# Performance work log

Hardware: AMD Instinct MI355X
Metric: run time of the kernel (lower is better)

The kernel has to match this reference:

```python
import jax, jax.numpy as jnp
import numpy as np

B, Q, C, H, W, E, HID_ATT, HID_MLP, NUM_CLASSES, NUM_LABELS = 8, 64, 512, 16, 16, 512, 128, 512, 14, 64


def setup_inputs() -> dict:
    key = jax.random.key(0)
    ks = jax.random.split(key, 16)
    s = 0.02
    return {
        "feature": jax.random.normal(ks[0], (B, C, H, W), jnp.float32),
        "label_ids": jax.random.randint(ks[1], (B, Q), 0, NUM_LABELS),
        "query_table": jax.random.normal(ks[2], (NUM_LABELS, E), jnp.float32) * s,
        "W_film": jax.random.normal(ks[3], (E, 2 * C), jnp.float32) * s,
        "b_film": jnp.zeros((2 * C,), jnp.float32),
        "W_att_h": jax.random.normal(ks[4], (C, HID_ATT), jnp.float32) * s,
        "b_att_h": jnp.zeros((HID_ATT,), jnp.float32),
        "W_att_f": jax.random.normal(ks[5], (HID_ATT, 1), jnp.float32) * s,
        "b_att_f": jnp.zeros((1,), jnp.float32),
        "W_mlp1": jax.random.normal(ks[6], (C, HID_MLP), jnp.float32) * s,
        "b_mlp1": jnp.zeros((HID_MLP,), jnp.float32),
        "W_mlp2": jax.random.normal(ks[7], (HID_MLP, NUM_CLASSES), jnp.float32) * s,
        "b_mlp2": jnp.zeros((NUM_CLASSES,), jnp.float32),
    }


def gelu(x):
    return jax.nn.gelu(x, approximate=False)  # torch default GELU is exact erf


def reference(feature, label_ids, query_table, W_film, b_film, W_att_h, b_att_h,
              W_att_f, b_att_f, W_mlp1, b_mlp1, W_mlp2, b_mlp2):
    # query embedding lookup: (B, Q, E)
    qe = query_table[label_ids]
    # flatten spatial: (B, HW, C)
    f = feature.reshape(feature.shape[0], feature.shape[1], -1).transpose(0, 2, 1)
    # FiLM params from queries: (B, Q, 2C) -> gamma, beta (B, Q, C)
    gb = jnp.einsum("bqe,ec->bqc", qe, W_film) + b_film
    gamma, beta = jnp.split(gb, 2, axis=-1)
    # FiLM-modulated features: (B, Q, HW, C)
    film = f[:, None, :, :] * gamma[:, :, None, :] + beta[:, :, None, :]
    # local attention MLP -> sigmoid gate (B, Q, HW, 1)
    hidden = gelu(jnp.einsum("bqnc,ch->bqnh", film, W_att_h) + b_att_h)
    attn = jax.nn.sigmoid(jnp.einsum("bqnh,ho->bqno", hidden, W_att_f) + b_att_f)
    # weighted sum pool over HW, normalized by attention mass
    pooled = (attn * film).sum(axis=2) / (attn.sum(axis=2) + 1e-8)  # (B, Q, C)
    # classification MLP
    logits = jnp.einsum("bqh,ho->bqo", gelu(jnp.einsum("bqc,ch->bqh", pooled, W_mlp1) + b_mlp1), W_mlp2) + b_mlp2
    return logits  # (B, Q, NUM_CLASSES)
```

## Files before the change

kernel.cpp:

```cpp
#include <hip/hip_runtime.h>
#include <hip/hip_bf16.h>

#define B_    8
#define Q_    64
#define C_    512
#define HW_   256
#define E_    512
#define HATT_ 128
#define HMLP_ 512
#define NCLS_ 14
#define NLAB_ 64

typedef unsigned short u16;
typedef unsigned int   u32;
typedef __attribute__((ext_vector_type(8))) short short8;
typedef __attribute__((ext_vector_type(4))) float f32x4;


__device__ __forceinline__ float gelu_fast(float x) {
    const float ax = fabsf(x);
    const float t  = __builtin_amdgcn_rcpf(1.0f + 0.3275911f * ax);
    const float p  = t * (0.254829592f +
                     t * (-0.284496736f +
                     t * (1.421413741f +
                     t * (-1.453152027f +
                     t * 1.061405429f))));
    const float e  = __expf(-x * x);
    const float er = copysignf(1.0f - p * e, x);
    return 0.5f * x * (1.0f + er);
}
__device__ __forceinline__ float sigmoid_(float x) {
    return 1.0f / (1.0f + __expf(-x));
}
__device__ __forceinline__ u16 f2bf(float x) {
    u32 u = __float_as_uint(x);
    u32 r = (u + 0x7fffu + ((u >> 16) & 1u)) >> 16;
    return (u16)r;
}
__device__ __forceinline__ float bf2f(u16 u) {
    return __uint_as_float(((u32)u) << 16);
}
__device__ __forceinline__ void gl2lds16(const void* gsrc, void* ldsdst) {
    __builtin_amdgcn_global_load_lds(
        (const __attribute__((address_space(1))) u32*)gsrc,
        (__attribute__((address_space(3))) u32*)ldsdst, 16, 0, 0);
}

__global__ __launch_bounds__(256) void prep_misc(
    const float* __restrict__ qt, const float* __restrict__ W_film,
    const float* __restrict__ feature, const float* __restrict__ W_mlp1,
    const int* __restrict__ label_ids,
    float* __restrict__ GBp, u16* __restrict__ W1bf, u16* __restrict__ fT,
    int* __restrict__ perm) {

    __shared__ __align__(16) char sm[16896];
    const int bid = blockIdx.x, t = threadIdx.x;

    if (bid < 256) {
        float* qrow = (float*)sm;
        const int l = bid >> 2, cq = bid & 3;
        if (t < 128) qrow[t] = qt[l * E_ + cq * 128 + t];
        __syncthreads();
        const float* wp = W_film + (size_t)(cq * 128) * 1024 + t * 4;
        f32x4 a = {0.f, 0.f, 0.f, 0.f};
        #pragma unroll 8
        for (int c = 0; c < 128; ++c) {
            const float4 w = *(const float4*)(wp + (size_t)c * 1024);
            const float q = qrow[c];
            a.x += q * w.x; a.y += q * w.y; a.z += q * w.z; a.w += q * w.w;
        }
        *(f32x4*)&GBp[(size_t)bid * 1024 + t * 4] = a;
    } else if (bid < 512) {
        float (*tile)[65] = (float(*)[65])sm;
        const int bb = bid - 256;
        const int b = bb >> 5, c0 = ((bb >> 2) & 7) * 64, n0 = (bb & 3) * 64;
        const float* fb = feature + (size_t)b * C_ * HW_;
        const int cl = t >> 2, nq = t & 3;
        #pragma unroll
        for (int i = 0; i < 4; ++i) {
            float4 v = *(const float4*)&fb[(c0 + cl) * HW_ + n0 + nq * 16 + i * 4];
            tile[cl][nq * 16 + i * 4 + 0] = v.x;
            tile[cl][nq * 16 + i * 4 + 1] = v.y;
            tile[cl][nq * 16 + i * 4 + 2] = v.z;
            tile[cl][nq * 16 + i * 4 + 3] = v.w;
        }
        __syncthreads();
        const int nl = t >> 2, cqq = t & 3;
        u16 pk[16];
        #pragma unroll
        for (int k = 0; k < 16; ++k) pk[k] = f2bf(tile[cqq * 16 + k][nl]);
        u16* dst = fT + (size_t)(b * HW_ + n0 + nl) * C_ + c0 + cqq * 16;
        *(uint4*)dst       = *(uint4*)pk;
        *(uint4*)(dst + 8) = *(uint4*)(pk + 8);
    } else if (bid < 576) {
        const int b2 = bid - 512;
        #pragma unroll
        for (int k = 0; k < 2; ++k) {
            const int idx = (b2 * 512 + k * 256 + t) * 8;
            float4 v0 = *(const float4*)&W_mlp1[idx];
            float4 v1 = *(const float4*)&W_mlp1[idx + 4];
            u16 pk[8] = {f2bf(v0.x), f2bf(v0.y), f2bf(v0.z), f2bf(v0.w),
                         f2bf(v1.x), f2bf(v1.y), f2bf(v1.z), f2bf(v1.w)};
            *(uint4*)&W1bf[idx] = *(uint4*)pk;
        }
    } else {
        int* cnt = (int*)sm;
        if (t < 64) cnt[t] = 0;
        __syncthreads();
        const int l0 = label_ids[t], l1 = label_ids[t + 256];
        atomicAdd(&cnt[l0], 1);
        atomicAdd(&cnt[l1], 1);
        __syncthreads();
        if (t == 0) {
            int run = 0;
            for (int i = 0; i < 64; ++i) { const int c = cnt[i]; cnt[i] = run; run += c; }
        }
        __syncthreads();
        const int p0 = atomicAdd(&cnt[l0], 1);
        perm[p0] = t | (l0 << 16);
        const int p1 = atomicAdd(&cnt[l1], 1);
        perm[p1] = (t + 256) | (l1 << 16);
    }
}

__global__ __launch_bounds__(256) void prep_wg(
    const float* __restrict__ b_film, const float* __restrict__ W_att_h,
    const float* __restrict__ GBp,
    float* __restrict__ Gl, float* __restrict__ Bl,
    u16* __restrict__ WgT, float* __restrict__ Dlp) {

    __shared__ float g_s[128], b_s[128], dred[256];
    const int bid = blockIdx.x, t = threadIdx.x;
    const int l = bid >> 2, cq = bid & 3;

    if (t < 128) {
        const int c = cq * 128 + t;
        float g = b_film[c], be = b_film[512 + c];
        #pragma unroll
        for (int j = 0; j < 4; ++j) {
            g  += GBp[(size_t)(l * 4 + j) * 1024 + c];
            be += GBp[(size_t)(l * 4 + j) * 1024 + 512 + c];
        }
        g_s[t] = g; b_s[t] = be;
        Gl[l * C_ + c] = g;
        Bl[l * C_ + c] = be;
    }
    __syncthreads();

    const int h = t & 127, ch = t >> 7;
    const int s = cq * 2 + ch;
    char* dst = (char*)WgT + (size_t)l * 131072 + s * 16384 + h * 128;
    float dl = 0.f;
    #pragma unroll
    for (int g = 0; g < 8; ++g) {
        u16 pk[8];
        #pragma unroll
        for (int j = 0; j < 8; ++j) {
            const int cl = ch * 64 + g * 8 + j;
            const float w = W_att_h[(size_t)(cq * 128 + cl) * HATT_ + h];
            pk[j] = f2bf(g_s[cl] * w);
            dl += b_s[cl] * w;
        }
        *(uint4*)(dst + ((g ^ (h & 7)) * 16)) = *(uint4*)pk;
    }
    dred[t] = dl;
    __syncthreads();
    if (t < 128)
        Dlp[(size_t)(l * 4 + cq) * 128 + t] = dred[t] + dred[128 + t];
}

__global__ __launch_bounds__(512, 4) void attn_gemm(
    const float* __restrict__ W_att_f, const float* __restrict__ b_att_f,
    const float* __restrict__ b_att_h, const float* __restrict__ Dlp,
    const int*   __restrict__ perm,    const u16* __restrict__ WgT,
    const u16*   __restrict__ fT,
    float* __restrict__ pP, float* __restrict__ pA) {

    __shared__ __align__(16) char Ash[32768];
    __shared__ __align__(16) char Bsh[16384];
    __shared__ float d_s[HATT_];
    __shared__ float wf_s[HATT_];
    __shared__ float attn_part[2][HW_];
    __shared__ float attn_s[HW_];

    const int t = threadIdx.x;
    const int srank = (blockIdx.x & 7) * 64 + (blockIdx.x >> 3);
    const int pe = perm[srank];
    const int bq = pe & 0xffff, l = pe >> 16;
    const int b = bq >> 6;

    if (t < HATT_) {
        d_s[t] = b_att_h[t]
               + Dlp[(size_t)(l * 4 + 0) * 128 + t]
               + Dlp[(size_t)(l * 4 + 1) * 128 + t]
               + Dlp[(size_t)(l * 4 + 2) * 128 + t]
               + Dlp[(size_t)(l * 4 + 3) * 128 + t];
        wf_s[t] = W_att_f[t];
    }

    const u16* fTb = fT + (size_t)b * HW_ * C_;
    const u16* Wl  = WgT + (size_t)l * 65536;

    const int an  = t >> 3;
    const int asl = (t & 7) ^ (an & 7);

    #define STAGE(s_) {                                                       \
        _Pragma("unroll")                                                     \
        for (int it = 0; it < 4; ++it)                                        \
            gl2lds16(fTb + (size_t)(it * 64 + an) * C_ + (s_) * 64 + asl * 8, \
                     Ash + (it * 512 + t) * 16);                              \
        _Pragma("unroll")                                                     \
        for (int it = 0; it < 2; ++it)                                        \
            gl2lds16(Wl + (size_t)(s_) * 8192 + (size_t)(it * 512 + t) * 8,   \
                     Bsh + (it * 512 + t) * 16);                              \
    }

    const int lane = t & 63, w = t >> 6;
    const int wm = w >> 1, wc = w & 1;
    const int lr = lane & 15, lk = lane >> 4;

    const f32x4 zero = {0.f, 0.f, 0.f, 0.f};
    f32x4 acc[4][4];
    #pragma unroll
    for (int mi = 0; mi < 4; ++mi)
        #pragma unroll
        for (int ni = 0; ni < 4; ++ni) acc[mi][ni] = zero;

    STAGE(0);
    __syncthreads();

    for (int s = 0; s < 8; ++s) {
        #pragma unroll
        for (int ks = 0; ks < 2; ++ks) {
            const int slot = ks * 4 + lk;
            short8 af[4], bf[4];
            #pragma unroll
            for (int mi = 0; mi < 4; ++mi) {
                const int nl = wm * 64 + mi * 16 + lr;
                af[mi] = *(const short8*)(Ash + nl * 128 + ((slot ^ (nl & 7)) * 16));
            }
            #pragma unroll
            for (int ni = 0; ni < 4; ++ni) {
                const int h = wc * 64 + ni * 16 + lr;
                bf[ni] = *(const short8*)(Bsh + h * 128 + ((slot ^ (h & 7)) * 16));
            }
            #pragma unroll
            for (int mi = 0; mi < 4; ++mi)
                #pragma unroll
                for (int ni = 0; ni < 4; ++ni)
                    acc[mi][ni] = __builtin_amdgcn_mfma_f32_16x16x32_bf16(
                        af[mi], bf[ni], acc[mi][ni], 0, 0, 0);
        }
        if (s < 7) {
            __syncthreads();
            STAGE(s + 1);
        }
        __syncthreads();
    }

    #pragma unroll
    for (int mi = 0; mi < 4; ++mi) {
        #pragma unroll
        for (int j = 0; j < 4; ++j) {
            float sum = 0.f;
            #pragma unroll
            for (int ni = 0; ni < 4; ++ni) {
                const int h = wc * 64 + ni * 16 + lr;
                sum += gelu_fast(acc[mi][ni][j] + d_s[h]) * wf_s[h];
            }
            sum += __shfl_xor(sum, 1);
            sum += __shfl_xor(sum, 2);
            sum += __shfl_xor(sum, 4);
            sum += __shfl_xor(sum, 8);
            if (lr == 0) attn_part[wc][wm * 64 + mi * 16 + lk * 4 + j] = sum;
        }
    }
    __syncthreads();
    if (t < HW_)
        attn_s[t] = sigmoid_(attn_part[0][t] + attn_part[1][t] + b_att_f[0]);
    __syncthreads();
    if (t < 64) {
        float a = attn_s[t] + attn_s[t + 64] + attn_s[t + 128] + attn_s[t + 192];
        #pragma unroll
        for (int m = 1; m < 64; m <<= 1) a += __shfl_xor(a, m);
        if (t == 0) pA[bq] = a;
    }

    float* pred = (float*)Ash;
    {
        const int ng = t >> 7, cb = (t & 127) * 4;
        const u16* fp = fTb + cb;
        f32x4 p = zero;
        #pragma unroll 8
        for (int n = ng * 64; n < ng * 64 + 64; ++n) {
            const uint2 v = *(const uint2*)(fp + (size_t)n * C_);
            const float a = attn_s[n];
            p.x += a * __uint_as_float(v.x << 16);
            p.y += a * __uint_as_float(v.x & 0xffff0000u);
            p.z += a * __uint_as_float(v.y << 16);
            p.w += a * __uint_as_float(v.y & 0xffff0000u);
        }
        *(f32x4*)&pred[ng * 512 + cb] = p;
    }
    __syncthreads();
    pP[(size_t)bq * C_ + t] = pred[t] + pred[512 + t] + pred[1024 + t] + pred[1536 + t];
}

__global__ __launch_bounds__(512) void mlp_head(
    const int*   __restrict__ label_ids,
    const float* __restrict__ Gl, const float* __restrict__ Bl,
    const float* __restrict__ b_mlp1, const float* __restrict__ W_mlp2,
    const float* __restrict__ b_mlp2, const float* __restrict__ pP,
    const float* __restrict__ pA,     const u16* __restrict__ W1bf,
    float* __restrict__ out) {

    __shared__ float pooled_s[2][C_];
    __shared__ float zred[2][2][HMLP_];
    __shared__ float z_s[2][HMLP_];
    __shared__ float red_s[32 * NCLS_];

    const int t = threadIdx.x;
    const int bq0 = blockIdx.x * 2;

    {
        const int bqi = t >> 8, cc = (t & 255) * 2;
        const int bq = bq0 + bqi, l = label_ids[bq];
        const float A = pA[bq];
        const float inv = 1.0f / (A + 1e-8f);
        #pragma unroll
        for (int i = 0; i < 2; ++i) {
            const int c = cc + i;
            const float p = pP[(size_t)bq * C_ + c];
            pooled_s[bqi][c] = (Gl[l * C_ + c] * p + Bl[l * C_ + c] * A) * inv;
        }
    }
    __syncthreads();

    {
        const int hp = t & 255, cg = t >> 8;
        float z00 = 0.f, z01 = 0.f, z10 = 0.f, z11 = 0.f;
        const u16* wp = W1bf + hp * 2;
        #pragma unroll 8
        for (int c = cg * 256; c < cg * 256 + 256; ++c) {
            const u32 v = *(const u32*)(wp + (size_t)c * HMLP_);
            const float w0 = __uint_as_float(v << 16);
            const float w1 = __uint_as_float(v & 0xffff0000u);
            const float pa = pooled_s[0][c], pb = pooled_s[1][c];
            z00 += pa * w0; z01 += pa * w1;
            z10 += pb * w0; z11 += pb * w1;
        }
        float2 a0 = {z00, z01}, a1 = {z10, z11};
        *(float2*)&zred[cg][0][hp * 2] = a0;
        *(float2*)&zred[cg][1][hp * 2] = a1;
    }
    __syncthreads();
    {
        const int bqi = t >> 8, h2 = (t & 255) * 2;
        #pragma unroll
        for (int i = 0; i < 2; ++i) {
            const int h = h2 + i;
            z_s[bqi][h] = gelu_fast(zred[0][bqi][h] + zred[1][bqi][h] + b_mlp1[h]);
        }
    }
    __syncthreads();

    #pragma unroll
    for (int bqi = 0; bqi < 2; ++bqi) {
        if (t < 448) {
            const int o = t % 14, seg = t / 14;
            float s = 0.f;
            #pragma unroll
            for (int k = 0; k < 16; ++k) {
                const int h = seg * 16 + k;
                s += z_s[bqi][h] * W_mlp2[h * NCLS_ + o];
            }
            red_s[seg * NCLS_ + o] = s;
        }
        __syncthreads();
        if (t < NCLS_) {
            float s = b_mlp2[t];
            #pragma unroll
            for (int seg = 0; seg < 32; ++seg) s += red_s[seg * NCLS_ + t];
            out[(bq0 + bqi) * NCLS_ + t] = s;
        }
        __syncthreads();
    }
}

extern "C" void kernel_launch(void* const* d_in, const int* in_sizes, int n_in,
                              void* d_out, int out_size, void* d_ws, size_t ws_size,
                              hipStream_t stream) {
    const float* feature   = (const float*)d_in[0];
    const int*   label_ids = (const int*)  d_in[1];
    const float* qt        = (const float*)d_in[2];
    const float* W_film    = (const float*)d_in[3];
    const float* b_film    = (const float*)d_in[4];
    const float* W_att_h   = (const float*)d_in[5];
    const float* b_att_h   = (const float*)d_in[6];
    const float* W_att_f   = (const float*)d_in[7];
    const float* b_att_f   = (const float*)d_in[8];
    const float* W_mlp1    = (const float*)d_in[9];
    const float* b_mlp1    = (const float*)d_in[10];
    const float* W_mlp2    = (const float*)d_in[11];
    const float* b_mlp2    = (const float*)d_in[12];
    float* out = (float*)d_out;

    char* wsb   = (char*)d_ws;
    float* GBp  = (float*)wsb;
    float* pP   = (float*)wsb;
    float* pA   = (float*)(wsb + 1048576);
    int*   perm = (int*)  (wsb + 1050624);
    float* Dlp  = (float*)(wsb + 1052672);
    float* Gl   = (float*)(wsb + 1183744);
    float* Bl   = (float*)(wsb + 1314816);
    u16*   W1bf = (u16*)  (wsb + 1445888);
    u16*   fTp  = (u16*)  (wsb + 1970176);
    u16*   WgT  = (u16*)  (wsb + 4067328);

    hipLaunchKernelGGL(prep_misc, dim3(577), dim3(256), 0, stream,
                       qt, W_film, feature, W_mlp1, label_ids,
                       GBp, W1bf, fTp, perm);
    hipLaunchKernelGGL(prep_wg, dim3(256), dim3(256), 0, stream,
                       b_film, W_att_h, GBp, Gl, Bl, WgT, Dlp);
    hipLaunchKernelGGL(attn_gemm, dim3(512), dim3(512), 0, stream,
                       W_att_f, b_att_f, b_att_h, Dlp, perm, WgT, fTp, pP, pA);
    hipLaunchKernelGGL(mlp_head, dim3(256), dim3(512), 0, stream,
                       label_ids, Gl, Bl, b_mlp1, W_mlp2, b_mlp2,
                       pP, pA, W1bf, out);
}
```

Before: 67.94 us.

## Double-buffer attention GEMM LDS tiles with 32-wide K stages

Splits the K dimension into 16 stages of 32 instead of 8 stages of 64 and double-buffers the A and B LDS tiles. The next stage's global-to-LDS copy is issued before the current stage's MFMAs, so loads can overlap compute and one barrier per stage is dropped. The weight pre-pack kernel is rewritten to the matching 64-byte row layout with a new XOR swizzle. This adds more barriers overall and smaller per-stage work, and the new swizzle may change LDS bank-conflict behaviour.

```diff
diff --git a/kernel.cpp b/kernel.cpp
--- a/kernel.cpp
+++ b/kernel.cpp
@@ -148,20 +148,24 @@
     __syncthreads();
 
     const int h = t & 127, ch = t >> 7;
-    const int s = cq * 2 + ch;
-    char* dst = (char*)WgT + (size_t)l * 131072 + s * 16384 + h * 128;
+    const int hswz = (h >> 1) & 3;
     float dl = 0.f;
     #pragma unroll
-    for (int g = 0; g < 8; ++g) {
-        u16 pk[8];
-        #pragma unroll
-        for (int j = 0; j < 8; ++j) {
-            const int cl = ch * 64 + g * 8 + j;
-            const float w = W_att_h[(size_t)(cq * 128 + cl) * HATT_ + h];
-            pk[j] = f2bf(g_s[cl] * w);
-            dl += b_s[cl] * w;
-        }
-        *(uint4*)(dst + ((g ^ (h & 7)) * 16)) = *(uint4*)pk;
+    for (int sl = 0; sl < 2; ++sl) {
+        const int ss = cq * 4 + ch * 2 + sl;
+        char* dst = (char*)WgT + (size_t)l * 131072 + ss * 8192 + h * 64;
+        #pragma unroll
+        for (int g = 0; g < 4; ++g) {
+            u16 pk[8];
+            #pragma unroll
+            for (int j = 0; j < 8; ++j) {
+                const int cl = ch * 64 + sl * 32 + g * 8 + j;
+                const float w = W_att_h[(size_t)(cq * 128 + cl) * HATT_ + h];
+                pk[j] = f2bf(g_s[cl] * w);
+                dl += b_s[cl] * w;
+            }
+            *(uint4*)(dst + ((g ^ hswz) * 16)) = *(uint4*)pk;
+        }
     }
     dred[t] = dl;
     __syncthreads();
@@ -176,8 +180,8 @@
     const u16*   __restrict__ fT,
     float* __restrict__ pP, float* __restrict__ pA) {
 
-    __shared__ __align__(16) char Ash[32768];
-    __shared__ __align__(16) char Bsh[16384];
+    __shared__ __align__(16) char Ash[2][16384];
+    __shared__ __align__(16) char Bsh[2][8192];
     __shared__ float d_s[HATT_];
     __shared__ float wf_s[HATT_];
     __shared__ float attn_part[2][HW_];
@@ -201,18 +205,17 @@
     const u16* fTb = fT + (size_t)b * HW_ * C_;
     const u16* Wl  = WgT + (size_t)l * 65536;
 
-    const int an  = t >> 3;
-    const int asl = (t & 7) ^ (an & 7);
+    const int an0 = t >> 2;
+    const int asl0 = (t & 3) ^ ((an0 >> 1) & 3);
 
     #define STAGE(s_) {                                                       \
         _Pragma("unroll")                                                     \
-        for (int it = 0; it < 4; ++it)                                        \
-            gl2lds16(fTb + (size_t)(it * 64 + an) * C_ + (s_) * 64 + asl * 8, \
-                     Ash + (it * 512 + t) * 16);                              \
-        _Pragma("unroll")                                                     \
         for (int it = 0; it < 2; ++it)                                        \
-            gl2lds16(Wl + (size_t)(s_) * 8192 + (size_t)(it * 512 + t) * 8,   \
-                     Bsh + (it * 512 + t) * 16);                              \
+            gl2lds16(fTb + (size_t)(it * 128 + an0) * C_ + (s_) * 32          \
+                         + asl0 * 8,                                          \
+                     &Ash[(s_) & 1][(it * 512 + t) * 16]);                    \
+        gl2lds16(Wl + (size_t)(s_) * 4096 + (size_t)t * 8,                    \
+                 &Bsh[(s_) & 1][t * 16]);                                     \
     }
 
     const int lane = t & 63, w = t >> 6;
@@ -229,32 +232,28 @@
     STAGE(0);
     __syncthreads();
 
-    for (int s = 0; s < 8; ++s) {
-        #pragma unroll
-        for (int ks = 0; ks < 2; ++ks) {
-            const int slot = ks * 4 + lk;
-            short8 af[4], bf[4];
+    #pragma unroll 2
+    for (int s = 0; s < 16; ++s) {
+        if (s < 15) STAGE(s + 1);
+        const char* Ab = Ash[s & 1];
+        const char* Bb = Bsh[s & 1];
+        short8 af[4], bf[4];
+        #pragma unroll
+        for (int mi = 0; mi < 4; ++mi) {
+            const int nl = wm * 64 + mi * 16 + lr;
+            af[mi] = *(const short8*)(Ab + nl * 64 + ((lk ^ ((nl >> 1) & 3)) * 16));
+        }
+        #pragma unroll
+        for (int ni = 0; ni < 4; ++ni) {
+            const int h = wc * 64 + ni * 16 + lr;
+            bf[ni] = *(const short8*)(Bb + h * 64 + ((lk ^ ((h >> 1) & 3)) * 16));
+        }
+        #pragma unroll
+        for (int mi = 0; mi < 4; ++mi)
             #pragma unroll
-            for (int mi = 0; mi < 4; ++mi) {
-                const int nl = wm * 64 + mi * 16 + lr;
-                af[mi] = *(const short8*)(Ash + nl * 128 + ((slot ^ (nl & 7)) * 16));
-            }
-            #pragma unroll
-            for (int ni = 0; ni < 4; ++ni) {
-                const int h = wc * 64 + ni * 16 + lr;
-                bf[ni] = *(const short8*)(Bsh + h * 128 + ((slot ^ (h & 7)) * 16));
-            }
-            #pragma unroll
-            for (int mi = 0; mi < 4; ++mi)
-                #pragma unroll
-                for (int ni = 0; ni < 4; ++ni)
-                    acc[mi][ni] = __builtin_amdgcn_mfma_f32_16x16x32_bf16(
-                        af[mi], bf[ni], acc[mi][ni], 0, 0, 0);
-        }
-        if (s < 7) {
-            __syncthreads();
-            STAGE(s + 1);
-        }
+            for (int ni = 0; ni < 4; ++ni)
+                acc[mi][ni] = __builtin_amdgcn_mfma_f32_16x16x32_bf16(
+                    af[mi], bf[ni], acc[mi][ni], 0, 0, 0);
         __syncthreads();
     }
 
```

After: 68.77 us. Within noise of the previous version (+1.2%).
